# Performance work log

Hardware: AMD Instinct MI355X
Metric: run time of the kernel (lower is better)

Reference implementation:

```python
import jax, jax.numpy as jnp
import numpy as np

N = 100000
E = 3200000


def gcn_conv(x, src, dst, W, b):
    """PyG GCNConv: symmetric-normalized aggregation with self-loops.
    src/dst already include self-loop edges. Messages flow src -> dst.
    """
    h = x @ W  # [N, F_out]
    # degree over destination index (includes self-loops), per gcn_norm
    deg = jax.ops.segment_sum(jnp.ones_like(dst, dtype=h.dtype), dst, num_segments=N)
    dinv = jnp.where(deg > 0, jax.lax.rsqrt(deg), 0.0)
    norm = dinv[src] * dinv[dst]  # [E+N]
    msg = h[src] * norm[:, None]  # gather + scale
    out = jax.ops.segment_sum(msg, dst, num_segments=N)  # scatter-add
    return out + b


def setup_inputs() -> dict:
    key = jax.random.key(0)
    k1, k2, k3, k4, k5, k6 = jax.random.split(key, 6)
    x = jax.random.normal(k1, (N, 3), dtype=jnp.float32)
    edge_index = jax.random.randint(k2, (2, E), 0, N, dtype=jnp.int64)
    # Glorot-style init for GCN weights, zero bias (PyG defaults)
    W1 = jax.random.normal(k3, (3, 16), dtype=jnp.float32) * (1.0 / np.sqrt(3))
    b1 = jnp.zeros((16,), dtype=jnp.float32)
    W2 = jax.random.normal(k4, (16, 1), dtype=jnp.float32) * (1.0 / np.sqrt(16))
    b2 = jnp.zeros((1,), dtype=jnp.float32)
    return {"x": x, "edge_index": edge_index, "W1": W1, "b1": b1, "W2": W2, "b2": b2}


def reference(x, edge_index, W1, b1, W2, b2):
    # add self-loops once (both layers use the same augmented graph)
    loops = jnp.arange(N, dtype=edge_index.dtype)
    src = jnp.concatenate([edge_index[0], loops])
    dst = jnp.concatenate([edge_index[1], loops])
    h = gcn_conv(x, src, dst, W1, b1)
    h = jax.nn.relu(h)
    h = gcn_conv(h, src, dst, W2, b2)
    return jax.nn.sigmoid(h)
```

## Files before the change

kernel.cpp:

```cpp
#include <hip/hip_runtime.h>
#include <math.h>


#define NPB 256
#define SHIFT 8
#define NB_MAX 512
#define SPLIT 8
#define T1 512
#define EPT 16

#define FSCALE 1024.0f
#define FBIAS  8192
#define FMASK  0x1FFFFFu

static __device__ __forceinline__ long long load_idx(const void* edges, long long pos, int is64) {
    if (is64) return ((const long long*)edges)[pos];
    return (long long)((const int*)edges)[pos];
}

static __device__ __forceinline__ unsigned long long pack3(float x, float y, float z) {
    unsigned long long e0 = (unsigned)(__float2int_rn(x * FSCALE) + FBIAS);
    unsigned long long e1 = (unsigned)(__float2int_rn(y * FSCALE) + FBIAS);
    unsigned long long e2 = (unsigned)(__float2int_rn(z * FSCALE) + FBIAS);
    return e0 | (e1 << 21) | (e2 << 42);
}

__global__ void k_zero_cursor(int* cursor, int nb, const int* e32, int* flag) {
    int i = blockIdx.x * blockDim.x + threadIdx.x;
    if (i < nb) cursor[i] = 0;
    if (i == 0) {
        int is64 = 1;
        for (int k = 0; k < 16; ++k)
            if (e32[2 * k + 1] != 0) { is64 = 0; break; }
        *flag = is64;
    }
}

__global__ void k_bin(const void* edges, const int* __restrict__ flag,
                      int* __restrict__ cursor, unsigned int* __restrict__ bin,
                      long long E, int nb, int cap) {
    __shared__ int hist[NB_MAX];
    __shared__ int base[NB_MAX];
    const int tid = threadIdx.x;
    for (int b = tid; b < nb; b += T1) hist[b] = 0;
    __syncthreads();

    const int is64 = *flag;
    const long long start = (long long)blockIdx.x * ((long long)T1 * EPT);
    unsigned es[EPT], ed[EPT];
    int rank[EPT];

    if (is64) {
        const long long* e64 = (const long long*)edges;
#pragma unroll
        for (int j = 0; j < EPT; ++j) {
            long long e = start + j * T1 + tid;
            if (e < E) { es[j] = (unsigned)e64[e]; ed[j] = (unsigned)e64[E + e]; }
            else ed[j] = 0xFFFFFFFFu;
        }
    } else {
        const int* e32 = (const int*)edges;
#pragma unroll
        for (int j = 0; j < EPT; ++j) {
            long long e = start + j * T1 + tid;
            if (e < E) { es[j] = (unsigned)e32[e]; ed[j] = (unsigned)e32[E + e]; }
            else ed[j] = 0xFFFFFFFFu;
        }
    }

#pragma unroll
    for (int j = 0; j < EPT; ++j)
        if (ed[j] != 0xFFFFFFFFu)
            rank[j] = atomicAdd(&hist[ed[j] >> SHIFT], 1);
    __syncthreads();

    for (int b = tid; b < nb; b += T1) {
        int h = hist[b];
        base[b] = h ? atomicAdd(&cursor[b], h) : 0;
    }
    __syncthreads();

#pragma unroll
    for (int j = 0; j < EPT; ++j) {
        if (ed[j] == 0xFFFFFFFFu) continue;
        int bk = (int)(ed[j] >> SHIFT);
        int off = base[bk] + rank[j];
        if (off < cap)
            bin[(long long)bk * cap + off] = ((ed[j] & (NPB - 1)) << 17) | es[j];
    }
}

static __device__ __forceinline__ void sub_range(int cnt, int sub, int* lo, int* hi) {
    int l = (int)(((long long)cnt * sub / SPLIT) & ~3LL);
    int h = (sub == SPLIT - 1) ? cnt : (int)(((long long)cnt * (sub + 1) / SPLIT) & ~3LL);
    *lo = l; *hi = h;
}

__global__ void k_degP(const unsigned int* __restrict__ bin, const int* __restrict__ cursor,
                       int* __restrict__ part, int cap) {
    __shared__ int dcnt[NPB];
    const int tid = threadIdx.x;
    dcnt[tid] = 0;
    __syncthreads();
    const int bk = blockIdx.x >> 3;
    const int sub = blockIdx.x & (SPLIT - 1);
    const int cnt = min(cursor[bk], cap);
    int lo, hi; sub_range(cnt, sub, &lo, &hi);
    const unsigned int* bp = bin + (long long)bk * cap;
    const int len = hi - lo, nvec = len >> 2;
    const uint4* bp4 = (const uint4*)(bp + lo);
    for (int v = tid; v < nvec; v += NPB) {
        uint4 q = bp4[v];
        atomicAdd(&dcnt[q.x >> 17], 1);
        atomicAdd(&dcnt[q.y >> 17], 1);
        atomicAdd(&dcnt[q.z >> 17], 1);
        atomicAdd(&dcnt[q.w >> 17], 1);
    }
    for (int k = lo + (nvec << 2) + tid; k < hi; k += NPB)
        atomicAdd(&dcnt[bp[k] >> 17], 1);
    __syncthreads();
    part[(long long)blockIdx.x * NPB + tid] = dcnt[tid];
}

__global__ void k_degC(const int* __restrict__ part, const float* __restrict__ x,
                       float* __restrict__ dinv, float4* __restrict__ xs, int n) {
    const int tid = threadIdx.x;
    const int bk = blockIdx.x;
    const int i = bk * NPB + tid;
    if (i >= n) return;
    int degE = 0;
#pragma unroll
    for (int s = 0; s < SPLIT; ++s)
        degE += part[(long long)(bk * SPLIT + s) * NPB + tid];
    float di = rsqrtf((float)degE + 1.0f);
    dinv[i] = di;
    xs[i] = make_float4(x[3 * i] * di, x[3 * i + 1] * di, x[3 * i + 2] * di, (float)degE);
}

__global__ void k_agg1P(const unsigned int* __restrict__ bin, const int* __restrict__ cursor,
                        const float4* __restrict__ xs, unsigned long long* __restrict__ part,
                        int cap) {
    __shared__ unsigned long long acc[NPB];
    const int tid = threadIdx.x;
    acc[tid] = 0ull;
    __syncthreads();
    const int bk = blockIdx.x >> 3;
    const int sub = blockIdx.x & (SPLIT - 1);
    const int cnt = min(cursor[bk], cap);
    int lo, hi; sub_range(cnt, sub, &lo, &hi);
    const unsigned int* bp = bin + (long long)bk * cap;
    const int len = hi - lo, nvec = len >> 2;
    const uint4* bp4 = (const uint4*)(bp + lo);
    for (int v = tid; v < nvec; v += NPB) {
        uint4 q = bp4[v];
        float4 v0 = xs[q.x & 0x1FFFFu];
        float4 v1 = xs[q.y & 0x1FFFFu];
        float4 v2 = xs[q.z & 0x1FFFFu];
        float4 v3 = xs[q.w & 0x1FFFFu];
        atomicAdd(&acc[q.x >> 17], pack3(v0.x, v0.y, v0.z));
        atomicAdd(&acc[q.y >> 17], pack3(v1.x, v1.y, v1.z));
        atomicAdd(&acc[q.z >> 17], pack3(v2.x, v2.y, v2.z));
        atomicAdd(&acc[q.w >> 17], pack3(v3.x, v3.y, v3.z));
    }
    for (int k = lo + (nvec << 2) + tid; k < hi; k += NPB) {
        unsigned p = bp[k];
        float4 v = xs[p & 0x1FFFFu];
        atomicAdd(&acc[p >> 17], pack3(v.x, v.y, v.z));
    }
    __syncthreads();
    part[(long long)blockIdx.x * NPB + tid] = acc[tid];
}

__global__ void k_agg1C(const unsigned long long* __restrict__ part,
                        const float* __restrict__ dinv, const float4* __restrict__ xs,
                        const float* __restrict__ W1, const float* __restrict__ b1,
                        const float* __restrict__ W2, float* __restrict__ gs, int n) {
    const int tid = threadIdx.x;
    const int bk = blockIdx.x;
    const int i = bk * NPB + tid;
    if (i >= n) return;
    int f0 = 0, f1 = 0, f2 = 0;
#pragma unroll
    for (int s = 0; s < SPLIT; ++s) {
        unsigned long long p = part[(long long)(bk * SPLIT + s) * NPB + tid];
        f0 += (int)(p & FMASK);
        f1 += (int)((p >> 21) & FMASK);
        f2 += (int)((p >> 42) & FMASK);
    }
    float4 self = xs[i];
    int degE = (int)self.w;
    const float inv = 1.0f / FSCALE;
    float a0 = (float)(f0 - FBIAS * degE) * inv + self.x;
    float a1 = (float)(f1 - FBIAS * degE) * inv + self.y;
    float a2 = (float)(f2 - FBIAS * degE) * inv + self.z;
    float di = dinv[i];
    a0 *= di; a1 *= di; a2 *= di;
    float g = 0.0f;
#pragma unroll
    for (int c = 0; c < 16; ++c) {
        float h = fmaf(a0, W1[c], fmaf(a1, W1[16 + c], fmaf(a2, W1[32 + c], b1[c])));
        h = fmaxf(h, 0.0f);
        g = fmaf(h, W2[c], g);
    }
    gs[i] = g * di;
}

__global__ void k_agg2P(const unsigned int* __restrict__ bin, const int* __restrict__ cursor,
                        const float* __restrict__ gs, float* __restrict__ part, int cap) {
    __shared__ float acc[NPB];
    const int tid = threadIdx.x;
    acc[tid] = 0.0f;
    __syncthreads();
    const int bk = blockIdx.x >> 3;
    const int sub = blockIdx.x & (SPLIT - 1);
    const int cnt = min(cursor[bk], cap);
    int lo, hi; sub_range(cnt, sub, &lo, &hi);
    const unsigned int* bp = bin + (long long)bk * cap;
    const int len = hi - lo, nvec = len >> 2;
    const uint4* bp4 = (const uint4*)(bp + lo);
    for (int v = tid; v < nvec; v += NPB) {
        uint4 q = bp4[v];
        float g0 = gs[q.x & 0x1FFFFu];
        float g1 = gs[q.y & 0x1FFFFu];
        float g2 = gs[q.z & 0x1FFFFu];
        float g3 = gs[q.w & 0x1FFFFu];
        atomicAdd(&acc[q.x >> 17], g0);
        atomicAdd(&acc[q.y >> 17], g1);
        atomicAdd(&acc[q.z >> 17], g2);
        atomicAdd(&acc[q.w >> 17], g3);
    }
    for (int k = lo + (nvec << 2) + tid; k < hi; k += NPB) {
        unsigned p = bp[k];
        atomicAdd(&acc[p >> 17], gs[p & 0x1FFFFu]);
    }
    __syncthreads();
    part[(long long)blockIdx.x * NPB + tid] = acc[tid];
}

__global__ void k_agg2C(const float* __restrict__ part, const float* __restrict__ dinv,
                        const float* __restrict__ gs, const float* __restrict__ b2,
                        float* __restrict__ out, int n) {
    const int tid = threadIdx.x;
    const int bk = blockIdx.x;
    const int i = bk * NPB + tid;
    if (i >= n) return;
    float acc = gs[i];
#pragma unroll
    for (int s = 0; s < SPLIT; ++s)
        acc += part[(long long)(bk * SPLIT + s) * NPB + tid];
    float z = dinv[i] * acc + b2[0];
    out[i] = 1.0f / (1.0f + expf(-z));
}

__global__ void k_detect(const int* e32, int* flag) {
    if (blockIdx.x == 0 && threadIdx.x == 0) {
        int is64 = 1;
        for (int k = 0; k < 16; ++k)
            if (e32[2 * k + 1] != 0) { is64 = 0; break; }
        *flag = is64;
    }
}
__global__ void f_init_deg(float* deg, int n) {
    int i = blockIdx.x * blockDim.x + threadIdx.x;
    if (i < n) deg[i] = 1.0f;
}
__global__ void f_deg(const void* edges, const int* flag, float* deg, long long E) {
    int is64 = *flag;
    long long e = (long long)blockIdx.x * blockDim.x + threadIdx.x;
    if (e < E) atomicAdd(&deg[load_idx(edges, E + e, is64)], 1.0f);
}
__global__ void f_dinv_xs(const float* x, const float* deg, float* dinv, float4* xs,
                          float4* agg3, int n) {
    int i = blockIdx.x * blockDim.x + threadIdx.x;
    if (i < n) {
        float di = rsqrtf(deg[i]);
        dinv[i] = di;
        float4 v = make_float4(x[3 * i] * di, x[3 * i + 1] * di, x[3 * i + 2] * di, 0.0f);
        xs[i] = v; agg3[i] = v;
    }
}
__global__ void f_edge1(const void* edges, const int* flag, const float4* xs,
                        float* agg3, long long E) {
    int is64 = *flag;
    long long e = (long long)blockIdx.x * blockDim.x + threadIdx.x;
    if (e < E) {
        long long s = load_idx(edges, e, is64);
        long long d = load_idx(edges, E + e, is64);
        float4 v = xs[s];
        atomicAdd(&agg3[4 * d + 0], v.x);
        atomicAdd(&agg3[4 * d + 1], v.y);
        atomicAdd(&agg3[4 * d + 2], v.z);
    }
}
__global__ void f_node1(const float* dinv, const float4* agg3, const float* W1,
                        const float* b1, const float* W2, float* gs, float* agg1, int n) {
    int i = blockIdx.x * blockDim.x + threadIdx.x;
    if (i < n) {
        float di = dinv[i];
        float4 a = agg3[i];
        float a0 = a.x * di, a1 = a.y * di, a2 = a.z * di;
        float g = 0.0f;
#pragma unroll
        for (int k = 0; k < 16; ++k) {
            float h = fmaf(a0, W1[k], fmaf(a1, W1[16 + k], fmaf(a2, W1[32 + k], b1[k])));
            h = fmaxf(h, 0.0f);
            g = fmaf(h, W2[k], g);
        }
        float v = g * di;
        gs[i] = v; agg1[i] = v;
    }
}
__global__ void f_edge2(const void* edges, const int* flag, const float* gs,
                        float* agg1, long long E) {
    int is64 = *flag;
    long long e = (long long)blockIdx.x * blockDim.x + threadIdx.x;
    if (e < E) atomicAdd(&agg1[load_idx(edges, E + e, is64)], gs[load_idx(edges, e, is64)]);
}
__global__ void f_final(const float* dinv, const float* agg1, const float* b2,
                        float* out, int n) {
    int i = blockIdx.x * blockDim.x + threadIdx.x;
    if (i < n) {
        float z = dinv[i] * agg1[i] + b2[0];
        out[i] = 1.0f / (1.0f + expf(-z));
    }
}

extern "C" void kernel_launch(void* const* d_in, const int* in_sizes, int n_in,
                              void* d_out, int out_size, void* d_ws, size_t ws_size,
                              hipStream_t stream) {
    const float* x  = (const float*)d_in[0];
    const void*  ei = d_in[1];
    const float* W1 = (const float*)d_in[2];
    const float* b1 = (const float*)d_in[3];
    const float* W2 = (const float*)d_in[4];
    const float* b2 = (const float*)d_in[5];
    float* out = (float*)d_out;

    const long long n = in_sizes[0] / 3;
    const long long E = in_sizes[1] / 2;

    const int T = 256;
    const int gN = (int)((n + T - 1) / T);
    const int gE = (int)((E + T - 1) / T);

    const int nb = (int)((n + NPB - 1) / NPB);
    long long capll = (E / nb) + (E / nb) / 8 + 256;
    const int cap = (int)((capll + 63) / 64 * 64);
    size_t need = n * sizeof(float4)
                + (size_t)nb * SPLIT * NPB * sizeof(float4)
                + (size_t)nb * cap * sizeof(int)
                + 2 * n * sizeof(float)
                + nb * sizeof(int) + 128;

    if (nb <= NB_MAX && n <= (1 << 17) && ws_size >= need) {
        char* p = (char*)d_ws;
        float4* xs   = (float4*)p;       p += n * sizeof(float4);
        char*  partb = p;                p += (size_t)nb * SPLIT * NPB * sizeof(float4);
        unsigned int* bin = (unsigned int*)p; p += (size_t)nb * cap * sizeof(int);
        float* dinv  = (float*)p;        p += n * sizeof(float);
        float* gs    = (float*)p;        p += n * sizeof(float);
        int*   cursor = (int*)p;         p += nb * sizeof(int);
        int*   flag  = (int*)p;

        const long long per_blk = (long long)T1 * EPT;
        const int gB = (int)((E + per_blk - 1) / per_blk);

        k_zero_cursor<<<(nb + T - 1) / T, T, 0, stream>>>(cursor, nb, (const int*)ei, flag);
        k_bin<<<gB, T1, 0, stream>>>(ei, flag, cursor, bin, E, nb, cap);
        k_degP<<<nb * SPLIT, NPB, 0, stream>>>(bin, cursor, (int*)partb, cap);
        k_degC<<<nb, NPB, 0, stream>>>((const int*)partb, x, dinv, xs, (int)n);
        k_agg1P<<<nb * SPLIT, NPB, 0, stream>>>(bin, cursor, xs, (unsigned long long*)partb, cap);
        k_agg1C<<<nb, NPB, 0, stream>>>((const unsigned long long*)partb, dinv, xs, W1, b1, W2, gs, (int)n);
        k_agg2P<<<nb * SPLIT, NPB, 0, stream>>>(bin, cursor, gs, (float*)partb, cap);
        k_agg2C<<<nb, NPB, 0, stream>>>((const float*)partb, dinv, gs, b2, out, (int)n);
    } else {
        char* p = (char*)d_ws;
        float*  deg  = (float*)p;  p += n * sizeof(float);
        float*  dinv = (float*)p;  p += n * sizeof(float);
        float4* xs   = (float4*)p; p += n * sizeof(float4);
        float4* agg3 = (float4*)p; p += n * sizeof(float4);
        float*  gs   = (float*)p;  p += n * sizeof(float);
        float*  agg1 = (float*)p;  p += n * sizeof(float);
        int*    flag = (int*)p;

        k_detect<<<1, 64, 0, stream>>>((const int*)ei, flag);
        f_init_deg<<<gN, T, 0, stream>>>(deg, (int)n);
        f_deg<<<gE, T, 0, stream>>>(ei, flag, deg, E);
        f_dinv_xs<<<gN, T, 0, stream>>>(x, deg, dinv, xs, agg3, (int)n);
        f_edge1<<<gE, T, 0, stream>>>(ei, flag, xs, (float*)agg3, E);
        f_node1<<<gN, T, 0, stream>>>(dinv, agg3, W1, b1, W2, gs, agg1, (int)n);
        f_edge2<<<gE, T, 0, stream>>>(ei, flag, gs, agg1, E);
        f_final<<<gN, T, 0, stream>>>(dinv, agg1, b2, out, (int)n);
    }
}
```

Baseline: 155.7 us.

## Build per-destination CSR via in-block scan and placement for gather aggregation

Adds a scan kernel that turns the per-sub-block destination counts into absolute offsets, and a placement kernel that writes each binned edge's source into a destination-sorted array (CSR-like). Both GCN layers then aggregate by gather: eight lanes per destination node sum neighbour features and reduce with shuffles, replacing the shared-memory atomic partial sums and the combine passes. This removes the atomic scatter and partial-buffer traffic but adds an extra pass that writes a second edge array, and it needs more workspace. If the workspace is too small, the previous path is still used.

```diff
diff --git a/kernel.cpp b/kernel.cpp
--- a/kernel.cpp
+++ b/kernel.cpp
@@ -120,6 +120,136 @@
         atomicAdd(&dcnt[bp[k] >> 17], 1);
     __syncthreads();
     part[(long long)blockIdx.x * NPB + tid] = dcnt[tid];
+}
+
+__global__ void k_scan(const int* __restrict__ part, const float* __restrict__ x,
+                       float* __restrict__ dinv, float4* __restrict__ xs,
+                       unsigned int* __restrict__ subStart, unsigned int* __restrict__ startAbs,
+                       int n, int cap) {
+    __shared__ int sc[NPB];
+    const int lid = threadIdx.x;
+    const int bk = blockIdx.x;
+    const int i = bk * NPB + lid;
+    int subOff[SPLIT];
+    int degE = 0;
+#pragma unroll
+    for (int s = 0; s < SPLIT; ++s) {
+        subOff[s] = degE;
+        degE += part[(long long)(bk * SPLIT + s) * NPB + lid];
+    }
+    sc[lid] = degE;
+    __syncthreads();
+    for (int off = 1; off < NPB; off <<= 1) {
+        int v = (lid >= off) ? sc[lid - off] : 0;
+        __syncthreads();
+        sc[lid] += v;
+        __syncthreads();
+    }
+    unsigned base = (unsigned)bk * (unsigned)cap + (unsigned)(sc[lid] - degE);
+#pragma unroll
+    for (int s = 0; s < SPLIT; ++s)
+        subStart[(long long)(bk * SPLIT + s) * NPB + lid] = base + (unsigned)subOff[s];
+    if (i < n) {
+        startAbs[i] = base;
+        float di = rsqrtf((float)degE + 1.0f);
+        dinv[i] = di;
+        xs[i] = make_float4(x[3 * i] * di, x[3 * i + 1] * di, x[3 * i + 2] * di, (float)degE);
+    }
+}
+
+__global__ void k_place(const unsigned int* __restrict__ bin, const int* __restrict__ cursor,
+                        const unsigned int* __restrict__ subStart,
+                        unsigned int* __restrict__ bin2, int cap) {
+    __shared__ unsigned int cnt[NPB];
+    const int tid = threadIdx.x;
+    cnt[tid] = subStart[(long long)blockIdx.x * NPB + tid];
+    __syncthreads();
+    const int bk = blockIdx.x >> 3;
+    const int sub = blockIdx.x & (SPLIT - 1);
+    const int cnt_b = min(cursor[bk], cap);
+    int lo, hi; sub_range(cnt_b, sub, &lo, &hi);
+    const unsigned int* bp = bin + (long long)bk * cap;
+    const int len = hi - lo, nvec = len >> 2;
+    const uint4* bp4 = (const uint4*)(bp + lo);
+    for (int v = tid; v < nvec; v += NPB) {
+        uint4 q = bp4[v];
+        unsigned p0 = atomicAdd(&cnt[q.x >> 17], 1u);
+        unsigned p1 = atomicAdd(&cnt[q.y >> 17], 1u);
+        unsigned p2 = atomicAdd(&cnt[q.z >> 17], 1u);
+        unsigned p3 = atomicAdd(&cnt[q.w >> 17], 1u);
+        bin2[p0] = q.x & 0x1FFFFu;
+        bin2[p1] = q.y & 0x1FFFFu;
+        bin2[p2] = q.z & 0x1FFFFu;
+        bin2[p3] = q.w & 0x1FFFFu;
+    }
+    for (int k = lo + (nvec << 2) + tid; k < hi; k += NPB) {
+        unsigned q = bp[k];
+        unsigned p = atomicAdd(&cnt[q >> 17], 1u);
+        bin2[p] = q & 0x1FFFFu;
+    }
+}
+
+__global__ void k_agg1F(const unsigned int* __restrict__ bin2,
+                        const unsigned int* __restrict__ startAbs,
+                        const float4* __restrict__ xs, const float* __restrict__ dinv,
+                        const float* __restrict__ W1, const float* __restrict__ b1,
+                        const float* __restrict__ W2, float* __restrict__ gs, int n) {
+    const int tid = threadIdx.x;
+    const int bk = blockIdx.x >> 3;
+    const int sub = blockIdx.x & 7;
+    const int g = tid >> 3, l = tid & 7;
+    const int i = bk * NPB + sub * 32 + g;
+    if (i >= n) return;
+    const unsigned start = startAbs[i];
+    const float4 self = xs[i];
+    const int degE = (int)self.w;
+    float a0 = 0.f, a1 = 0.f, a2 = 0.f;
+    for (int k = l; k < degE; k += 8) {
+        unsigned src = bin2[start + k];
+        float4 v = xs[src];
+        a0 += v.x; a1 += v.y; a2 += v.z;
+    }
+#pragma unroll
+    for (int m = 1; m < 8; m <<= 1) {
+        a0 += __shfl_xor(a0, m);
+        a1 += __shfl_xor(a1, m);
+        a2 += __shfl_xor(a2, m);
+    }
+    float di = dinv[i];
+    a0 = (a0 + self.x) * di; a1 = (a1 + self.y) * di; a2 = (a2 + self.z) * di;
+    float gsum = 0.f;
+#pragma unroll
+    for (int c = 0; c < 16; ++c) {
+        float h = fmaf(a0, W1[c], fmaf(a1, W1[16 + c], fmaf(a2, W1[32 + c], b1[c])));
+        h = fmaxf(h, 0.0f);
+        gsum = fmaf(h, W2[c], gsum);
+    }
+    if (l == 0) gs[i] = gsum * di;
+}
+
+__global__ void k_agg2F(const unsigned int* __restrict__ bin2,
+                        const unsigned int* __restrict__ startAbs,
+                        const float4* __restrict__ xs, const float* __restrict__ gs,
+                        const float* __restrict__ dinv, const float* __restrict__ b2,
+                        float* __restrict__ out, int n) {
+    const int tid = threadIdx.x;
+    const int bk = blockIdx.x >> 3;
+    const int sub = blockIdx.x & 7;
+    const int g = tid >> 3, l = tid & 7;
+    const int i = bk * NPB + sub * 32 + g;
+    if (i >= n) return;
+    const unsigned start = startAbs[i];
+    const int degE = (int)xs[i].w;
+    float acc = 0.f;
+    for (int k = l; k < degE; k += 8)
+        acc += gs[bin2[start + k]];
+#pragma unroll
+    for (int m = 1; m < 8; m <<= 1)
+        acc += __shfl_xor(acc, m);
+    if (l == 0) {
+        float z = dinv[i] * (acc + gs[i]) + b2[0];
+        out[i] = 1.0f / (1.0f + expf(-z));
+    }
 }
 
 __global__ void k_degC(const int* __restrict__ part, const float* __restrict__ x,
@@ -346,13 +476,44 @@
     const int nb = (int)((n + NPB - 1) / NPB);
     long long capll = (E / nb) + (E / nb) / 8 + 256;
     const int cap = (int)((capll + 63) / 64 * 64);
-    size_t need = n * sizeof(float4)
-                + (size_t)nb * SPLIT * NPB * sizeof(float4)
-                + (size_t)nb * cap * sizeof(int)
-                + 2 * n * sizeof(float)
-                + nb * sizeof(int) + 128;
-
-    if (nb <= NB_MAX && n <= (1 << 17) && ws_size >= need) {
+
+    size_t needNew = n * sizeof(float4)
+                   + (size_t)nb * SPLIT * NPB * sizeof(int)
+                   + (size_t)nb * SPLIT * NPB * sizeof(int)
+                   + (size_t)nb * cap * sizeof(int)
+                   + (size_t)nb * cap * sizeof(int)
+                   + 3 * n * sizeof(float)
+                   + nb * sizeof(int) + 128;
+    size_t needMid = n * sizeof(float4)
+                   + (size_t)nb * SPLIT * NPB * sizeof(float4)
+                   + (size_t)nb * cap * sizeof(int)
+                   + 2 * n * sizeof(float)
+                   + nb * sizeof(int) + 128;
+
+    if (nb <= NB_MAX && n <= (1 << 17) && ws_size >= needNew) {
+        char* p = (char*)d_ws;
+        float4* xs   = (float4*)p;            p += n * sizeof(float4);
+        int* cnts    = (int*)p;               p += (size_t)nb * SPLIT * NPB * sizeof(int);
+        unsigned int* subStart = (unsigned int*)p; p += (size_t)nb * SPLIT * NPB * sizeof(int);
+        unsigned int* bin  = (unsigned int*)p; p += (size_t)nb * cap * sizeof(int);
+        unsigned int* bin2 = (unsigned int*)p; p += (size_t)nb * cap * sizeof(int);
+        float* dinv  = (float*)p;             p += n * sizeof(float);
+        float* gs    = (float*)p;             p += n * sizeof(float);
+        unsigned int* startAbs = (unsigned int*)p; p += n * sizeof(int);
+        int*   cursor = (int*)p;              p += nb * sizeof(int);
+        int*   flag  = (int*)p;
+
+        const long long per_blk = (long long)T1 * EPT;
+        const int gB = (int)((E + per_blk - 1) / per_blk);
+
+        k_zero_cursor<<<(nb + T - 1) / T, T, 0, stream>>>(cursor, nb, (const int*)ei, flag);
+        k_bin<<<gB, T1, 0, stream>>>(ei, flag, cursor, bin, E, nb, cap);
+        k_degP<<<nb * SPLIT, NPB, 0, stream>>>(bin, cursor, cnts, cap);
+        k_scan<<<nb, NPB, 0, stream>>>(cnts, x, dinv, xs, subStart, startAbs, (int)n, cap);
+        k_place<<<nb * SPLIT, NPB, 0, stream>>>(bin, cursor, subStart, bin2, cap);
+        k_agg1F<<<nb * SPLIT, NPB, 0, stream>>>(bin2, startAbs, xs, dinv, W1, b1, W2, gs, (int)n);
+        k_agg2F<<<nb * SPLIT, NPB, 0, stream>>>(bin2, startAbs, xs, gs, dinv, b2, out, (int)n);
+    } else if (nb <= NB_MAX && n <= (1 << 17) && ws_size >= needMid) {
         char* p = (char*)d_ws;
         float4* xs   = (float4*)p;       p += n * sizeof(float4);
         char*  partb = p;                p += (size_t)nb * SPLIT * NPB * sizeof(float4);
```

Measured after the change: 169.5 us. +8.9%, slower.

## Fuse split partial-reduce and combine kernels into single per-bucket kernels

Applied to the files above, without the earlier changes.

Drops the SPLIT=8 partitioning of each destination bucket, so one 512-thread block now processes a whole bucket and does the per-node finalize in the same kernel. This removes three combine launches and the partial-sum buffer round trip through global memory. In exchange, the grid shrinks from nb*8 to nb blocks (about 391 blocks for roughly 256 CUs), which cuts parallelism and makes each block's serial edge loop about four times longer.

```diff
diff --git a/kernel.cpp b/kernel.cpp
--- a/kernel.cpp
+++ b/kernel.cpp
@@ -5,9 +5,9 @@
 #define NPB 256
 #define SHIFT 8
 #define NB_MAX 512
-#define SPLIT 8
 #define T1 512
 #define EPT 16
+#define T2 512
 
 #define FSCALE 1024.0f
 #define FBIAS  8192
@@ -25,7 +25,7 @@
     return e0 | (e1 << 21) | (e2 << 42);
 }
 
-__global__ void k_zero_cursor(int* cursor, int nb, const int* e32, int* flag) {
+__global__ void k_zf(int* cursor, int nb, const int* e32, int* flag) {
     int i = blockIdx.x * blockDim.x + threadIdx.x;
     if (i < nb) cursor[i] = 0;
     if (i == 0) {
@@ -90,68 +90,54 @@
     }
 }
 
-static __device__ __forceinline__ void sub_range(int cnt, int sub, int* lo, int* hi) {
-    int l = (int)(((long long)cnt * sub / SPLIT) & ~3LL);
-    int h = (sub == SPLIT - 1) ? cnt : (int)(((long long)cnt * (sub + 1) / SPLIT) & ~3LL);
-    *lo = l; *hi = h;
-}
-
-__global__ void k_degP(const unsigned int* __restrict__ bin, const int* __restrict__ cursor,
-                       int* __restrict__ part, int cap) {
+__global__ void k_degF(const unsigned int* __restrict__ bin, const int* __restrict__ cursor,
+                       const float* __restrict__ x, float* __restrict__ dinv,
+                       float4* __restrict__ xs, int cap, int n) {
     __shared__ int dcnt[NPB];
     const int tid = threadIdx.x;
-    dcnt[tid] = 0;
-    __syncthreads();
-    const int bk = blockIdx.x >> 3;
-    const int sub = blockIdx.x & (SPLIT - 1);
+    if (tid < NPB) dcnt[tid] = 0;
+    __syncthreads();
+    const int bk = blockIdx.x;
     const int cnt = min(cursor[bk], cap);
-    int lo, hi; sub_range(cnt, sub, &lo, &hi);
     const unsigned int* bp = bin + (long long)bk * cap;
-    const int len = hi - lo, nvec = len >> 2;
-    const uint4* bp4 = (const uint4*)(bp + lo);
-    for (int v = tid; v < nvec; v += NPB) {
+    const int nvec = cnt >> 2;
+    const uint4* bp4 = (const uint4*)bp;
+    for (int v = tid; v < nvec; v += T2) {
         uint4 q = bp4[v];
         atomicAdd(&dcnt[q.x >> 17], 1);
         atomicAdd(&dcnt[q.y >> 17], 1);
         atomicAdd(&dcnt[q.z >> 17], 1);
         atomicAdd(&dcnt[q.w >> 17], 1);
     }
-    for (int k = lo + (nvec << 2) + tid; k < hi; k += NPB)
+    for (int k = (nvec << 2) + tid; k < cnt; k += T2)
         atomicAdd(&dcnt[bp[k] >> 17], 1);
     __syncthreads();
-    part[(long long)blockIdx.x * NPB + tid] = dcnt[tid];
-}
-
-__global__ void k_degC(const int* __restrict__ part, const float* __restrict__ x,
-                       float* __restrict__ dinv, float4* __restrict__ xs, int n) {
-    const int tid = threadIdx.x;
-    const int bk = blockIdx.x;
-    const int i = bk * NPB + tid;
-    if (i >= n) return;
-    int degE = 0;
-#pragma unroll
-    for (int s = 0; s < SPLIT; ++s)
-        degE += part[(long long)(bk * SPLIT + s) * NPB + tid];
-    float di = rsqrtf((float)degE + 1.0f);
-    dinv[i] = di;
-    xs[i] = make_float4(x[3 * i] * di, x[3 * i + 1] * di, x[3 * i + 2] * di, (float)degE);
-}
-
-__global__ void k_agg1P(const unsigned int* __restrict__ bin, const int* __restrict__ cursor,
-                        const float4* __restrict__ xs, unsigned long long* __restrict__ part,
-                        int cap) {
+    if (tid < NPB) {
+        const int i = bk * NPB + tid;
+        if (i < n) {
+            int degE = dcnt[tid];
+            float di = rsqrtf((float)degE + 1.0f);
+            dinv[i] = di;
+            xs[i] = make_float4(x[3 * i] * di, x[3 * i + 1] * di, x[3 * i + 2] * di, (float)degE);
+        }
+    }
+}
+
+__global__ void k_agg1FU(const unsigned int* __restrict__ bin, const int* __restrict__ cursor,
+                         const float4* __restrict__ xs, const float* __restrict__ dinv,
+                         const float* __restrict__ W1, const float* __restrict__ b1,
+                         const float* __restrict__ W2, float* __restrict__ gs,
+                         int cap, int n) {
     __shared__ unsigned long long acc[NPB];
     const int tid = threadIdx.x;
-    acc[tid] = 0ull;
-    __syncthreads();
-    const int bk = blockIdx.x >> 3;
-    const int sub = blockIdx.x & (SPLIT - 1);
+    if (tid < NPB) acc[tid] = 0ull;
+    __syncthreads();
+    const int bk = blockIdx.x;
     const int cnt = min(cursor[bk], cap);
-    int lo, hi; sub_range(cnt, sub, &lo, &hi);
     const unsigned int* bp = bin + (long long)bk * cap;
-    const int len = hi - lo, nvec = len >> 2;
-    const uint4* bp4 = (const uint4*)(bp + lo);
-    for (int v = tid; v < nvec; v += NPB) {
+    const int nvec = cnt >> 2;
+    const uint4* bp4 = (const uint4*)bp;
+    for (int v = tid; v < nvec; v += T2) {
         uint4 q = bp4[v];
         float4 v0 = xs[q.x & 0x1FFFFu];
         float4 v1 = xs[q.y & 0x1FFFFu];
@@ -162,94 +148,73 @@
         atomicAdd(&acc[q.z >> 17], pack3(v2.x, v2.y, v2.z));
         atomicAdd(&acc[q.w >> 17], pack3(v3.x, v3.y, v3.z));
     }
-    for (int k = lo + (nvec << 2) + tid; k < hi; k += NPB) {
+    for (int k = (nvec << 2) + tid; k < cnt; k += T2) {
         unsigned p = bp[k];
         float4 v = xs[p & 0x1FFFFu];
         atomicAdd(&acc[p >> 17], pack3(v.x, v.y, v.z));
     }
     __syncthreads();
-    part[(long long)blockIdx.x * NPB + tid] = acc[tid];
-}
-
-__global__ void k_agg1C(const unsigned long long* __restrict__ part,
-                        const float* __restrict__ dinv, const float4* __restrict__ xs,
-                        const float* __restrict__ W1, const float* __restrict__ b1,
-                        const float* __restrict__ W2, float* __restrict__ gs, int n) {
+    if (tid < NPB) {
+        const int i = bk * NPB + tid;
+        if (i < n) {
+            unsigned long long p = acc[tid];
+            int f0 = (int)(p & FMASK);
+            int f1 = (int)((p >> 21) & FMASK);
+            int f2 = (int)((p >> 42) & FMASK);
+            float4 self = xs[i];
+            int degE = (int)self.w;
+            const float inv = 1.0f / FSCALE;
+            float a0 = (float)(f0 - FBIAS * degE) * inv + self.x;
+            float a1 = (float)(f1 - FBIAS * degE) * inv + self.y;
+            float a2 = (float)(f2 - FBIAS * degE) * inv + self.z;
+            float di = dinv[i];
+            a0 *= di; a1 *= di; a2 *= di;
+            float g = 0.0f;
+#pragma unroll
+            for (int c = 0; c < 16; ++c) {
+                float h = fmaf(a0, W1[c], fmaf(a1, W1[16 + c], fmaf(a2, W1[32 + c], b1[c])));
+                h = fmaxf(h, 0.0f);
+                g = fmaf(h, W2[c], g);
+            }
+            gs[i] = g * di;
+        }
+    }
+}
+
+__global__ void k_agg2FU(const unsigned int* __restrict__ bin, const int* __restrict__ cursor,
+                         const float* __restrict__ gs, const float* __restrict__ dinv,
+                         const float* __restrict__ b2, float* __restrict__ out,
+                         int cap, int n) {
+    __shared__ float facc[NPB];
     const int tid = threadIdx.x;
+    if (tid < NPB) facc[tid] = 0.0f;
+    __syncthreads();
     const int bk = blockIdx.x;
-    const int i = bk * NPB + tid;
-    if (i >= n) return;
-    int f0 = 0, f1 = 0, f2 = 0;
-#pragma unroll
-    for (int s = 0; s < SPLIT; ++s) {
-        unsigned long long p = part[(long long)(bk * SPLIT + s) * NPB + tid];
-        f0 += (int)(p & FMASK);
-        f1 += (int)((p >> 21) & FMASK);
-        f2 += (int)((p >> 42) & FMASK);
-    }
-    float4 self = xs[i];
-    int degE = (int)self.w;
-    const float inv = 1.0f / FSCALE;
-    float a0 = (float)(f0 - FBIAS * degE) * inv + self.x;
-    float a1 = (float)(f1 - FBIAS * degE) * inv + self.y;
-    float a2 = (float)(f2 - FBIAS * degE) * inv + self.z;
-    float di = dinv[i];
-    a0 *= di; a1 *= di; a2 *= di;
-    float g = 0.0f;
-#pragma unroll
-    for (int c = 0; c < 16; ++c) {
-        float h = fmaf(a0, W1[c], fmaf(a1, W1[16 + c], fmaf(a2, W1[32 + c], b1[c])));
-        h = fmaxf(h, 0.0f);
-        g = fmaf(h, W2[c], g);
-    }
-    gs[i] = g * di;
-}
-
-__global__ void k_agg2P(const unsigned int* __restrict__ bin, const int* __restrict__ cursor,
-                        const float* __restrict__ gs, float* __restrict__ part, int cap) {
-    __shared__ float acc[NPB];
-    const int tid = threadIdx.x;
-    acc[tid] = 0.0f;
-    __syncthreads();
-    const int bk = blockIdx.x >> 3;
-    const int sub = blockIdx.x & (SPLIT - 1);
     const int cnt = min(cursor[bk], cap);
-    int lo, hi; sub_range(cnt, sub, &lo, &hi);
     const unsigned int* bp = bin + (long long)bk * cap;
-    const int len = hi - lo, nvec = len >> 2;
-    const uint4* bp4 = (const uint4*)(bp + lo);
-    for (int v = tid; v < nvec; v += NPB) {
+    const int nvec = cnt >> 2;
+    const uint4* bp4 = (const uint4*)bp;
+    for (int v = tid; v < nvec; v += T2) {
         uint4 q = bp4[v];
         float g0 = gs[q.x & 0x1FFFFu];
         float g1 = gs[q.y & 0x1FFFFu];
         float g2 = gs[q.z & 0x1FFFFu];
         float g3 = gs[q.w & 0x1FFFFu];
-        atomicAdd(&acc[q.x >> 17], g0);
-        atomicAdd(&acc[q.y >> 17], g1);
-        atomicAdd(&acc[q.z >> 17], g2);
-        atomicAdd(&acc[q.w >> 17], g3);
-    }
-    for (int k = lo + (nvec << 2) + tid; k < hi; k += NPB) {
-        unsigned p = bp[k];
-        atomicAdd(&acc[p >> 17], gs[p & 0x1FFFFu]);
-    }
-    __syncthreads();
-    part[(long long)blockIdx.x * NPB + tid] = acc[tid];
-}
-
-__global__ void k_agg2C(const float* __restrict__ part, const float* __restrict__ dinv,
-                        const float* __restrict__ gs, const float* __restrict__ b2,
-                        float* __restrict__ out, int n) {
-    const int tid = threadIdx.x;
-    const int bk = blockIdx.x;
-    const int i = bk * NPB + tid;
-    if (i >= n) return;
-    float acc = gs[i];
-#pragma unroll
-    for (int s = 0; s < SPLIT; ++s)
-        acc += part[(long long)(bk * SPLIT + s) * NPB + tid];
-    float z = dinv[i] * acc + b2[0];
-    out[i] = 1.0f / (1.0f + expf(-z));
+        atomicAdd(&facc[q.x >> 17], g0);
+        atomicAdd(&facc[q.y >> 17], g1);
+        atomicAdd(&facc[q.z >> 17], g2);
+        atomicAdd(&facc[q.w >> 17], g3);
+    }
+    for (int k = (nvec << 2) + tid; k < cnt; k += T2)
+        atomicAdd(&facc[bp[k] >> 17], gs[bp[k] & 0x1FFFFu]);
+    __syncthreads();
+    if (tid < NPB) {
+        const int i = bk * NPB + tid;
+        if (i < n) {
+            float z = dinv[i] * (facc[tid] + gs[i]) + b2[0];
+            out[i] = 1.0f / (1.0f + expf(-z));
+        }
+    }
 }
 
 __global__ void k_detect(const int* e32, int* flag) {
@@ -346,33 +311,29 @@
     const int nb = (int)((n + NPB - 1) / NPB);
     long long capll = (E / nb) + (E / nb) / 8 + 256;
     const int cap = (int)((capll + 63) / 64 * 64);
+
     size_t need = n * sizeof(float4)
-                + (size_t)nb * SPLIT * NPB * sizeof(float4)
                 + (size_t)nb * cap * sizeof(int)
                 + 2 * n * sizeof(float)
                 + nb * sizeof(int) + 128;
 
     if (nb <= NB_MAX && n <= (1 << 17) && ws_size >= need) {
         char* p = (char*)d_ws;
-        float4* xs   = (float4*)p;       p += n * sizeof(float4);
-        char*  partb = p;                p += (size_t)nb * SPLIT * NPB * sizeof(float4);
+        float4* xs   = (float4*)p;            p += n * sizeof(float4);
         unsigned int* bin = (unsigned int*)p; p += (size_t)nb * cap * sizeof(int);
-        float* dinv  = (float*)p;        p += n * sizeof(float);
-        float* gs    = (float*)p;        p += n * sizeof(float);
-        int*   cursor = (int*)p;         p += nb * sizeof(int);
+        float* dinv  = (float*)p;             p += n * sizeof(float);
+        float* gs    = (float*)p;             p += n * sizeof(float);
+        int*   cursor = (int*)p;              p += nb * sizeof(int);
         int*   flag  = (int*)p;
 
         const long long per_blk = (long long)T1 * EPT;
         const int gB = (int)((E + per_blk - 1) / per_blk);
 
-        k_zero_cursor<<<(nb + T - 1) / T, T, 0, stream>>>(cursor, nb, (const int*)ei, flag);
+        k_zf<<<(nb + T - 1) / T, T, 0, stream>>>(cursor, nb, (const int*)ei, flag);
         k_bin<<<gB, T1, 0, stream>>>(ei, flag, cursor, bin, E, nb, cap);
-        k_degP<<<nb * SPLIT, NPB, 0, stream>>>(bin, cursor, (int*)partb, cap);
-        k_degC<<<nb, NPB, 0, stream>>>((const int*)partb, x, dinv, xs, (int)n);
-        k_agg1P<<<nb * SPLIT, NPB, 0, stream>>>(bin, cursor, xs, (unsigned long long*)partb, cap);
-        k_agg1C<<<nb, NPB, 0, stream>>>((const unsigned long long*)partb, dinv, xs, W1, b1, W2, gs, (int)n);
-        k_agg2P<<<nb * SPLIT, NPB, 0, stream>>>(bin, cursor, gs, (float*)partb, cap);
-        k_agg2C<<<nb, NPB, 0, stream>>>((const float*)partb, dinv, gs, b2, out, (int)n);
+        k_degF<<<nb, T2, 0, stream>>>(bin, cursor, x, dinv, xs, cap, (int)n);
+        k_agg1FU<<<nb, T2, 0, stream>>>(bin, cursor, xs, dinv, W1, b1, W2, gs, cap, (int)n);
+        k_agg2FU<<<nb, T2, 0, stream>>>(bin, cursor, gs, dinv, b2, out, cap, (int)n);
     } else {
         char* p = (char*)d_ws;
         float*  deg  = (float*)p;  p += n * sizeof(float);
```

Measured after the change: 151.1 us. 1.03x faster.
